# Kernel optimization log

Measured on AMD Instinct MI355X. Metric: run time of the kernel, lower is better.

The kernel has to match this reference:

```python
import jax, jax.numpy as jnp
import numpy as np

HOPS = 2
BN_EPS = 1e-5


def _glorot(key, shape):
    fan_in = shape[-2]
    bound = 1.0 / np.sqrt(fan_in)
    return jax.random.uniform(key, shape, jnp.float32, -bound, bound)


def setup_inputs() -> dict:
    key = jax.random.key(0)
    ks = jax.random.split(key, 12)
    n, e = 50000, 800000
    in_c, hid, out_c = 128, 96, 64
    x = jax.random.normal(ks[0], (n, in_c), jnp.float32)
    edge_index = jax.random.randint(ks[1], (2, e), 0, n, jnp.int32)
    # MixHopLayer 0: hops+1 linears in_c -> hid (stacked)
    conv0_W = _glorot(ks[2], (HOPS + 1, in_c, hid))
    conv0_b = jnp.zeros((HOPS + 1, hid), jnp.float32)
    # MixHopLayer 1: hops+1 linears hid*(hops+1) -> out_c
    conv1_W = _glorot(ks[3], (HOPS + 1, hid * (HOPS + 1), out_c))
    conv1_b = jnp.zeros((HOPS + 1, out_c), jnp.float32)
    # BatchNorm1d(hid*(hops+1)) eval-mode params/buffers
    w = hid * (HOPS + 1)
    bn_gamma = jnp.ones((w,), jnp.float32)
    bn_beta = jnp.zeros((w,), jnp.float32)
    bn_mean = 0.1 * jax.random.normal(ks[4], (w,), jnp.float32)
    bn_var = jnp.ones((w,), jnp.float32) + 0.1 * jax.random.uniform(ks[5], (w,))
    # final projection out_c*(hops+1) -> out_c
    fp_W = _glorot(ks[6], (out_c * (HOPS + 1), out_c))
    fp_b = jnp.zeros((out_c,), jnp.float32)
    return dict(x=x, edge_index=edge_index, conv0_W=conv0_W, conv0_b=conv0_b,
                conv1_W=conv1_W, conv1_b=conv1_b, bn_gamma=bn_gamma, bn_beta=bn_beta,
                bn_mean=bn_mean, bn_var=bn_var, fp_W=fp_W, fp_b=fp_b)


def _gcn_norm(edge_index, n):
    # PyG gcn_norm with add_self_loops=True, improved=False, symmetric norm.
    row, col = edge_index[0], edge_index[1]
    loop = jnp.arange(n, dtype=edge_index.dtype)
    row = jnp.concatenate([row, loop])
    col = jnp.concatenate([col, loop])
    deg = jax.ops.segment_sum(jnp.ones_like(col, jnp.float32), col, num_segments=n)
    dinv = jnp.where(deg > 0, jax.lax.rsqrt(deg), 0.0)
    w = dinv[row] * dinv[col]
    return row, col, w


def _spmm_adj_t(row, col, w, x, n):
    # adj_t = SparseTensor(row=col, col=row, value=w): out[col] += w * x[row]
    return jax.ops.segment_sum(w[:, None] * x[row], col, num_segments=n)


def _mixhop_layer(x, W, b, row, col, w, n):
    xs = [x @ W[0] + b[0]]
    for j in range(1, HOPS + 1):
        xj = x @ W[j] + b[j]
        for _ in range(j):
            xj = _spmm_adj_t(row, col, w, xj, n)
        xs.append(xj)
    return jnp.concatenate(xs, axis=1)


def reference(x, edge_index, conv0_W, conv0_b, conv1_W, conv1_b,
              bn_gamma, bn_beta, bn_mean, bn_var, fp_W, fp_b):
    n = x.shape[0]
    row, col, w = _gcn_norm(edge_index, n)
    h = _mixhop_layer(x, conv0_W, conv0_b, row, col, w, n)
    # BatchNorm1d (eval) + ReLU; dropout is identity in eval
    h = bn_gamma * (h - bn_mean) * jax.lax.rsqrt(bn_var + BN_EPS) + bn_beta
    h = jax.nn.relu(h)
    h = _mixhop_layer(h, conv1_W, conv1_b, row, col, w, n)
    return h @ fp_W + fp_b
```

## Files before the change

kernel.cpp:

```cpp
#include <hip/hip_runtime.h>

#define IN_C 128
#define HID 96
#define OUT_C 64
#define W0C 288
#define W1C 192
#define CAP 5120
#define EPB 4096

typedef __bf16 bf16x8v __attribute__((ext_vector_type(8)));
typedef float  f32x4v  __attribute__((ext_vector_type(4)));


__global__ void k_zero(int* __restrict__ p, int n) {
    int i = blockIdx.x * blockDim.x + threadIdx.x;
    if (i < n) p[i] = 0;
}

__global__ void k_count(const int* __restrict__ col, int* __restrict__ counts, int e) {
    int i = blockIdx.x * blockDim.x + threadIdx.x;
    if (i < e) atomicAdd(&counts[col[i]], 1);
}

__global__ void k_block_sum(const int* __restrict__ counts, int* __restrict__ bsums,
                            float* __restrict__ dinv, int n) {
    __shared__ int s[256];
    int i = blockIdx.x * 256 + threadIdx.x;
    int v = (i < n) ? counts[i] : 0;
    if (i < n) dinv[i] = rsqrtf((float)(v + 1));
    s[threadIdx.x] = v;
    __syncthreads();
    for (int off = 128; off > 0; off >>= 1) {
        if (threadIdx.x < (unsigned)off) s[threadIdx.x] += s[threadIdx.x + off];
        __syncthreads();
    }
    if (threadIdx.x == 0) bsums[blockIdx.x] = s[0];
}

__global__ void k_scan_bsums(int* __restrict__ bsums, int nb) {
    __shared__ int s[256];
    int v = ((int)threadIdx.x < nb) ? bsums[threadIdx.x] : 0;
    s[threadIdx.x] = v;
    __syncthreads();
    for (int off = 1; off < 256; off <<= 1) {
        int t = ((int)threadIdx.x >= off) ? s[threadIdx.x - off] : 0;
        __syncthreads();
        s[threadIdx.x] += t;
        __syncthreads();
    }
    if ((int)threadIdx.x < nb) bsums[threadIdx.x] = s[threadIdx.x] - v;
}

__global__ void k_row_ptr(const int* __restrict__ counts, const int* __restrict__ boffs,
                          int* __restrict__ row_ptr, int n) {
    __shared__ int s[256];
    int i = blockIdx.x * 256 + threadIdx.x;
    int v = (i < n) ? counts[i] : 0;
    s[threadIdx.x] = v;
    __syncthreads();
    for (int off = 1; off < 256; off <<= 1) {
        int t = ((int)threadIdx.x >= off) ? s[threadIdx.x - off] : 0;
        __syncthreads();
        s[threadIdx.x] += t;
        __syncthreads();
    }
    if (i < n) {
        row_ptr[i] = boffs[blockIdx.x] + s[threadIdx.x] - v;
        if (i == n - 1) row_ptr[n] = boffs[blockIdx.x] + s[threadIdx.x];
    }
}

__global__ __launch_bounds__(256) void k_binscatter(
        const int* __restrict__ row, const int* __restrict__ col,
        const int* __restrict__ row_ptr, int* __restrict__ bcur ,
        int2* __restrict__ binned, int e) {
    __shared__ int hist[256];
    __shared__ int base[256];
    int tid = threadIdx.x;
    int e0 = blockIdx.x * EPB;
    int cnt = min(EPB, e - e0);
    hist[tid] = 0;
    __syncthreads();
    int rr[16], cc[16], rk[16];
#pragma unroll
    for (int k = 0; k < 16; k++) {
        int idx = tid + k * 256;
        if (idx < cnt) {
            rr[k] = row[e0 + idx];
            cc[k] = col[e0 + idx];
            rk[k] = atomicAdd(&hist[cc[k] >> 8], 1);
        }
    }
    __syncthreads();
    {
        int h = hist[tid];
        if (h > 0) base[tid] = atomicAdd(&bcur[tid * 16], h);
    }
    __syncthreads();
#pragma unroll
    for (int k = 0; k < 16; k++) {
        int idx = tid + k * 256;
        if (idx < cnt) {
            int b = cc[k] >> 8;
            binned[row_ptr[b << 8] + base[b] + rk[k]] = make_int2(rr[k], cc[k]);
        }
    }
}

__global__ __launch_bounds__(256) void k_bucket_sort(
        const int2* __restrict__ binned, const int* __restrict__ row_ptr,
        const float* __restrict__ dinv,
        int* __restrict__ csr_src, float* __restrict__ csr_w, int n) {
    __shared__ int   s_src[CAP];
    __shared__ int   s_col[CAP];
    __shared__ int   s_ofs[256];
    __shared__ int   lcur[256];
    int tid = threadIdx.x;
    int node0 = blockIdx.x << 8;
    int nodeEnd = min(node0 + 256, n);
    int base = row_ptr[node0];
    int end  = row_ptr[nodeEnd];
    int cnt  = end - base;

    lcur[tid] = 0;
    __syncthreads();
    for (int t = tid; t < cnt; t += 256) {
        atomicAdd(&lcur[binned[base + t].x >> 8], 1);
    }
    __syncthreads();
    {
        int v = lcur[tid];
        s_ofs[tid] = v;
        __syncthreads();
        for (int o = 1; o < 256; o <<= 1) {
            int u = (tid >= o) ? s_ofs[tid - o] : 0;
            __syncthreads();
            s_ofs[tid] += u;
            __syncthreads();
        }
        lcur[tid] = s_ofs[tid] - v;
    }
    __syncthreads();
    for (int t = tid; t < cnt; t += 256) {
        int2 rc = binned[base + t];
        int pos = atomicAdd(&lcur[rc.x >> 8], 1);
        if (pos < CAP) {
            s_src[pos] = rc.x;
            s_col[pos] = rc.y;
        }
    }
    __syncthreads();
    {
        int node = node0 + tid;
        s_ofs[tid] = (node < n) ? (row_ptr[node] - base) : cnt;
        lcur[tid] = 0;
    }
    __syncthreads();
    int lim = min(cnt, CAP);
    for (int t = tid; t < lim; t += 256) {
        int r = s_src[t], c = s_col[t];
        int local = c - node0;
        int pos = s_ofs[local] + atomicAdd(&lcur[local], 1);
        csr_src[base + pos] = r;
        csr_w[base + pos]   = dinv[r] * dinv[c];
    }
}


__global__ void k_cvt_bf16(const float* __restrict__ src, __bf16* __restrict__ dst, int n8) {
    int i = blockIdx.x * blockDim.x + threadIdx.x;
    if (i >= n8) return;
    bf16x8v o;
#pragma unroll
    for (int q = 0; q < 8; q++) o[q] = (__bf16)src[i * 8 + q];
    *(bf16x8v*)(dst + (size_t)i * 8) = o;
}

__global__ void k_prep_all(const float* __restrict__ W0, const float* __restrict__ W1,
                           const float* __restrict__ Wf,
                           const float* __restrict__ gamma, const float* __restrict__ beta,
                           const float* __restrict__ mean, const float* __restrict__ var,
                           __bf16* __restrict__ w0t, __bf16* __restrict__ w1t,
                           __bf16* __restrict__ wft,
                           float* __restrict__ scale, float* __restrict__ shift) {
    const int T0 = 3 * IN_C * HID;
    const int T1 = 3 * W0C * OUT_C;
    const int T2 = W1C * OUT_C;
    int i = blockIdx.x * blockDim.x + threadIdx.x;
    if (i < T0) {
        int kn = IN_C * HID;
        int j = i / kn, r = i % kn;
        int k = r / HID, nn = r % HID;
        w0t[(size_t)j * kn + (size_t)nn * IN_C + k] = (__bf16)W0[i];
    } else if (i < T0 + T1) {
        int ii = i - T0;
        int kn = W0C * OUT_C;
        int j = ii / kn, r = ii % kn;
        int k = r / OUT_C, nn = r % OUT_C;
        w1t[(size_t)j * kn + (size_t)nn * W0C + k] = (__bf16)W1[ii];
    } else if (i < T0 + T1 + T2) {
        int ii = i - T0 - T1;
        int k = ii / OUT_C, nn = ii % OUT_C;
        wft[(size_t)nn * W1C + k] = (__bf16)Wf[ii];
    } else if (i < T0 + T1 + T2 + W0C) {
        int ii = i - T0 - T1 - T2;
        float s = gamma[ii] * rsqrtf(var[ii] + 1e-5f);
        scale[ii] = s;
        shift[ii] = beta[ii] - mean[ii] * s;
    }
}


__global__ __launch_bounds__(256) void k_mf_l0(
        const __bf16* __restrict__ xb, const __bf16* __restrict__ w0t ,
        const float* __restrict__ bias ,
        __bf16* __restrict__ h, __bf16* __restrict__ t12,
        const float* __restrict__ scale, const float* __restrict__ shift, int M) {
    const int RS = 104;
    __shared__ __bf16 tile[128 * RS];
    int tid = threadIdx.x;
    int wave = tid >> 6, lane = tid & 63;
    int ln = lane & 15, quad = lane >> 4;
    int j = blockIdx.y;
    int rowBase = blockIdx.x * 128;
    int waveRow = wave * 16;
    const __bf16* wjt = w0t + (size_t)j * HID * IN_C;
    f32x4v acc[2][6];
#pragma unroll
    for (int u = 0; u < 2; u++)
#pragma unroll
        for (int t = 0; t < 6; t++) acc[u][t] = (f32x4v){0.f, 0.f, 0.f, 0.f};
    const __bf16* arow0 = xb + (size_t)(rowBase + waveRow + ln) * IN_C + quad * 8;
    const __bf16* arow1 = arow0 + (size_t)64 * IN_C;
#pragma unroll
    for (int k = 0; k < 4; k++) {
        bf16x8v a0 = *(const bf16x8v*)(arow0 + k * 32);
        bf16x8v a1 = *(const bf16x8v*)(arow1 + k * 32);
#pragma unroll
        for (int c = 0; c < 6; c++) {
            bf16x8v b = *(const bf16x8v*)(wjt + (size_t)(c * 16 + ln) * IN_C + k * 32 + quad * 8);
            acc[0][c] = __builtin_amdgcn_mfma_f32_16x16x32_bf16(a0, b, acc[0][c], 0, 0, 0);
            acc[1][c] = __builtin_amdgcn_mfma_f32_16x16x32_bf16(a1, b, acc[1][c], 0, 0, 0);
        }
    }
    const float* bj = bias + j * HID;
    bool bn = (j == 0);
#pragma unroll
    for (int u = 0; u < 2; u++)
#pragma unroll
        for (int r = 0; r < 4; r++) {
            int lr = u * 64 + waveRow + quad * 4 + r;
#pragma unroll
            for (int c = 0; c < 6; c++) {
                int col = c * 16 + ln;
                float v = acc[u][c][r] + bj[col];
                if (bn) v = fmaxf(v * scale[col] + shift[col], 0.f);
                tile[lr * RS + col] = (__bf16)v;
            }
        }
    __syncthreads();
    __bf16* dst; int ld, c0;
    if (j == 0) { dst = h;   ld = W0C; c0 = 0; }
    else        { dst = t12; ld = 192; c0 = (j - 1) * 96; }
#pragma unroll
    for (int s = 0; s < 6; s++) {
        int idx = tid + s * 256;
        int r = idx / 12, c8 = idx % 12;
        int grow = rowBase + r;
        if (grow < M)
            *(bf16x8v*)(dst + (size_t)grow * ld + c0 + c8 * 8) =
                *(const bf16x8v*)(tile + r * RS + c8 * 8);
    }
}

__global__ __launch_bounds__(256) void k_mf_l1(
        const __bf16* __restrict__ hb, const __bf16* __restrict__ w1t ,
        const float* __restrict__ bias ,
        __bf16* __restrict__ g, __bf16* __restrict__ u12, int M) {
    const int RS = 72;
    __shared__ __bf16 tile[128 * RS];
    int tid = threadIdx.x;
    int wave = tid >> 6, lane = tid & 63;
    int ln = lane & 15, quad = lane >> 4;
    int j = blockIdx.y;
    int rowBase = blockIdx.x * 128;
    int waveRow = wave * 16;
    const __bf16* wjt = w1t + (size_t)j * OUT_C * W0C;
    f32x4v acc[2][4];
#pragma unroll
    for (int u = 0; u < 2; u++)
#pragma unroll
        for (int t = 0; t < 4; t++) acc[u][t] = (f32x4v){0.f, 0.f, 0.f, 0.f};
    const __bf16* arow0 = hb + (size_t)(rowBase + waveRow + ln) * W0C + quad * 8;
    const __bf16* arow1 = arow0 + (size_t)64 * W0C;
#pragma unroll
    for (int k = 0; k < 9; k++) {
        bf16x8v a0 = *(const bf16x8v*)(arow0 + k * 32);
        bf16x8v a1 = *(const bf16x8v*)(arow1 + k * 32);
#pragma unroll
        for (int c = 0; c < 4; c++) {
            bf16x8v b = *(const bf16x8v*)(wjt + (size_t)(c * 16 + ln) * W0C + k * 32 + quad * 8);
            acc[0][c] = __builtin_amdgcn_mfma_f32_16x16x32_bf16(a0, b, acc[0][c], 0, 0, 0);
            acc[1][c] = __builtin_amdgcn_mfma_f32_16x16x32_bf16(a1, b, acc[1][c], 0, 0, 0);
        }
    }
    const float* bj = bias + j * OUT_C;
#pragma unroll
    for (int u = 0; u < 2; u++)
#pragma unroll
        for (int r = 0; r < 4; r++) {
            int lr = u * 64 + waveRow + quad * 4 + r;
#pragma unroll
            for (int c = 0; c < 4; c++) {
                int col = c * 16 + ln;
                tile[lr * RS + col] = (__bf16)(acc[u][c][r] + bj[col]);
            }
        }
    __syncthreads();
    __bf16* dst; int ld, c0;
    if (j == 0) { dst = g;   ld = W1C; c0 = 0; }
    else        { dst = u12; ld = 128; c0 = (j - 1) * 64; }
#pragma unroll
    for (int s = 0; s < 4; s++) {
        int idx = tid + s * 256;
        int r = idx / 8, c8 = idx % 8;
        int grow = rowBase + r;
        if (grow < M)
            *(bf16x8v*)(dst + (size_t)grow * ld + c0 + c8 * 8) =
                *(const bf16x8v*)(tile + r * RS + c8 * 8);
    }
}

__global__ __launch_bounds__(256) void k_mf_fin(
        const __bf16* __restrict__ gb, const __bf16* __restrict__ wft ,
        const float* __restrict__ bias, float* __restrict__ out, int M) {
    const int RS = 68;
    __shared__ float tile[128 * RS];
    int tid = threadIdx.x;
    int wave = tid >> 6, lane = tid & 63;
    int ln = lane & 15, quad = lane >> 4;
    int rowBase = blockIdx.x * 128;
    int waveRow = wave * 16;
    f32x4v acc[2][4];
#pragma unroll
    for (int u = 0; u < 2; u++)
#pragma unroll
        for (int t = 0; t < 4; t++) acc[u][t] = (f32x4v){0.f, 0.f, 0.f, 0.f};
    const __bf16* arow0 = gb + (size_t)(rowBase + waveRow + ln) * W1C + quad * 8;
    const __bf16* arow1 = arow0 + (size_t)64 * W1C;
#pragma unroll
    for (int k = 0; k < 6; k++) {
        bf16x8v a0 = *(const bf16x8v*)(arow0 + k * 32);
        bf16x8v a1 = *(const bf16x8v*)(arow1 + k * 32);
#pragma unroll
        for (int c = 0; c < 4; c++) {
            bf16x8v b = *(const bf16x8v*)(wft + (size_t)(c * 16 + ln) * W1C + k * 32 + quad * 8);
            acc[0][c] = __builtin_amdgcn_mfma_f32_16x16x32_bf16(a0, b, acc[0][c], 0, 0, 0);
            acc[1][c] = __builtin_amdgcn_mfma_f32_16x16x32_bf16(a1, b, acc[1][c], 0, 0, 0);
        }
    }
#pragma unroll
    for (int u = 0; u < 2; u++)
#pragma unroll
        for (int r = 0; r < 4; r++) {
            int lr = u * 64 + waveRow + quad * 4 + r;
#pragma unroll
            for (int c = 0; c < 4; c++) {
                int col = c * 16 + ln;
                tile[lr * RS + col] = acc[u][c][r] + bias[col];
            }
        }
    __syncthreads();
#pragma unroll
    for (int s = 0; s < 8; s++) {
        int idx = tid + s * 256;
        int r = idx / 16, c4 = idx % 16;
        int grow = rowBase + r;
        if (grow < M)
            *(float4*)(out + (size_t)grow * OUT_C + c4 * 4) =
                *(const float4*)(tile + r * RS + c4 * 4);
    }
}

template <int C8, int NPB, bool BNRELU>
__global__ void k_spmm(const __bf16* __restrict__ xin, int ldx,
                       __bf16* __restrict__ xout, int ldo,
                       const int* __restrict__ row_ptr, const int* __restrict__ counts,
                       const int* __restrict__ csr_src, const float* __restrict__ csr_w,
                       const float* __restrict__ dinv, int n,
                       const float* __restrict__ scale, const float* __restrict__ shift,
                       int chan0) {
    int c8 = threadIdx.x % C8;
    int nl = threadIdx.x / C8;
    int node = blockIdx.x * NPB + nl;
    if (node >= n) return;
    float di = dinv[node];
    float lw = di * di;
    float acc[8];
    {
        bf16x8v v = *(const bf16x8v*)(xin + (size_t)node * ldx + c8 * 8);
#pragma unroll
        for (int q = 0; q < 8; q++) acc[q] = lw * (float)v[q];
    }
    int start = row_ptr[node];
    int cnt = counts[node];
    int k = 0;
    for (; k + 4 <= cnt; k += 4) {
        int s0 = csr_src[start + k + 0], s1 = csr_src[start + k + 1];
        int s2 = csr_src[start + k + 2], s3 = csr_src[start + k + 3];
        float w0 = csr_w[start + k + 0], w1 = csr_w[start + k + 1];
        float w2 = csr_w[start + k + 2], w3 = csr_w[start + k + 3];
        bf16x8v v0 = *(const bf16x8v*)(xin + (size_t)s0 * ldx + c8 * 8);
        bf16x8v v1 = *(const bf16x8v*)(xin + (size_t)s1 * ldx + c8 * 8);
        bf16x8v v2 = *(const bf16x8v*)(xin + (size_t)s2 * ldx + c8 * 8);
        bf16x8v v3 = *(const bf16x8v*)(xin + (size_t)s3 * ldx + c8 * 8);
#pragma unroll
        for (int q = 0; q < 8; q++)
            acc[q] += w0 * (float)v0[q] + w1 * (float)v1[q] +
                      w2 * (float)v2[q] + w3 * (float)v3[q];
    }
    for (; k < cnt; k++) {
        int src = csr_src[start + k];
        float w = csr_w[start + k];
        bf16x8v xv = *(const bf16x8v*)(xin + (size_t)src * ldx + c8 * 8);
#pragma unroll
        for (int q = 0; q < 8; q++) acc[q] += w * (float)xv[q];
    }
    bf16x8v o;
#pragma unroll
    for (int q = 0; q < 8; q++) {
        float v = acc[q];
        if (BNRELU) {
            int ch = chan0 + c8 * 8 + q;
            v = fmaxf(v * scale[ch] + shift[ch], 0.f);
        }
        o[q] = (__bf16)v;
    }
    *(bf16x8v*)(xout + (size_t)node * ldo + c8 * 8) = o;
}

template <int C8, int SPLIT, int NPB, bool BNA, bool BNB>
__global__ void k_spmm2(const __bf16* __restrict__ xin, int ldx,
                        __bf16* __restrict__ dstA, int ldA, int chanA,
                        __bf16* __restrict__ dstB, int ldB, int chanB,
                        const int* __restrict__ row_ptr, const int* __restrict__ counts,
                        const int* __restrict__ csr_src, const float* __restrict__ csr_w,
                        const float* __restrict__ dinv, int n,
                        const float* __restrict__ scale, const float* __restrict__ shift) {
    int c8 = threadIdx.x % C8;
    int nl = threadIdx.x / C8;
    int node = blockIdx.x * NPB + nl;
    if (node >= n) return;
    float di = dinv[node];
    float lw = di * di;
    float acc[8];
    {
        bf16x8v v = *(const bf16x8v*)(xin + (size_t)node * ldx + c8 * 8);
#pragma unroll
        for (int q = 0; q < 8; q++) acc[q] = lw * (float)v[q];
    }
    int start = row_ptr[node];
    int cnt = counts[node];
    int k = 0;
    for (; k + 4 <= cnt; k += 4) {
        int s0 = csr_src[start + k + 0], s1 = csr_src[start + k + 1];
        int s2 = csr_src[start + k + 2], s3 = csr_src[start + k + 3];
        float w0 = csr_w[start + k + 0], w1 = csr_w[start + k + 1];
        float w2 = csr_w[start + k + 2], w3 = csr_w[start + k + 3];
        bf16x8v v0 = *(const bf16x8v*)(xin + (size_t)s0 * ldx + c8 * 8);
        bf16x8v v1 = *(const bf16x8v*)(xin + (size_t)s1 * ldx + c8 * 8);
        bf16x8v v2 = *(const bf16x8v*)(xin + (size_t)s2 * ldx + c8 * 8);
        bf16x8v v3 = *(const bf16x8v*)(xin + (size_t)s3 * ldx + c8 * 8);
#pragma unroll
        for (int q = 0; q < 8; q++)
            acc[q] += w0 * (float)v0[q] + w1 * (float)v1[q] +
                      w2 * (float)v2[q] + w3 * (float)v3[q];
    }
    for (; k < cnt; k++) {
        int src = csr_src[start + k];
        float w = csr_w[start + k];
        bf16x8v xv = *(const bf16x8v*)(xin + (size_t)src * ldx + c8 * 8);
#pragma unroll
        for (int q = 0; q < 8; q++) acc[q] += w * (float)xv[q];
    }
    bool isA = c8 < SPLIT;
    __bf16* dst = isA ? dstA : dstB;
    int ld   = isA ? ldA : ldB;
    int lc8  = isA ? c8 : c8 - SPLIT;
    int chan = isA ? chanA : chanB;
    bool bn  = isA ? BNA : BNB;
    bf16x8v o;
#pragma unroll
    for (int q = 0; q < 8; q++) {
        float v = acc[q];
        if (bn) {
            int ch = chan + lc8 * 8 + q;
            v = fmaxf(v * scale[ch] + shift[ch], 0.f);
        }
        o[q] = (__bf16)v;
    }
    *(bf16x8v*)(dst + (size_t)node * ld + lc8 * 8) = o;
}


extern "C" void kernel_launch(void* const* d_in, const int* in_sizes, int n_in,
                              void* d_out, int out_size, void* d_ws, size_t ws_size,
                              hipStream_t stream) {
    const int n = in_sizes[0] / IN_C;
    const int e = in_sizes[1] / 2;

    const float* x    = (const float*)d_in[0];
    const int*   ei   = (const int*)d_in[1];
    const float* W0   = (const float*)d_in[2];
    const float* b0   = (const float*)d_in[3];
    const float* W1   = (const float*)d_in[4];
    const float* b1   = (const float*)d_in[5];
    const float* bn_g = (const float*)d_in[6];
    const float* bn_b = (const float*)d_in[7];
    const float* bn_m = (const float*)d_in[8];
    const float* bn_v = (const float*)d_in[9];
    const float* Wf   = (const float*)d_in[10];
    const float* bf   = (const float*)d_in[11];
    float* out = (float*)d_out;

    const int* e_row = ei;
    const int* e_col = ei + e;

    char* ws = (char*)d_ws;
    size_t off = 0;
    auto alloc = [&](size_t bytes) -> void* {
        void* p = ws + off;
        off += (bytes + 255) & ~(size_t)255;
        return p;
    };
    const int NP = n + 128;
    int*    counts  = (int*)alloc((size_t)(n + 256 * 16) * 4);
    int*    bcur    = counts + n;
    int*    row_ptr = (int*)alloc((size_t)(n + 1) * 4);
    int*    bsums   = (int*)alloc(256 * 4);
    float*  dinv    = (float*)alloc((size_t)n * 4);
    int2*   binned  = (int2*)alloc((size_t)e * 8);
    int*    csr_src = (int*)alloc((size_t)e * 4);
    float*  csr_w   = (float*)alloc((size_t)e * 4);
    float*  bnscale = (float*)alloc(W0C * 4);
    float*  bnshift = (float*)alloc(W0C * 4);
    __bf16* xb  = (__bf16*)alloc((size_t)NP * IN_C * 2);
    __bf16* w0t = (__bf16*)alloc((size_t)3 * HID * IN_C * 2);
    __bf16* w1t = (__bf16*)alloc((size_t)3 * OUT_C * W0C * 2);
    __bf16* wft = (__bf16*)alloc((size_t)OUT_C * W1C * 2);
    __bf16* t12 = (__bf16*)alloc((size_t)NP * 192 * 2);
    __bf16* tp  = (__bf16*)alloc((size_t)NP * HID * 2);
    __bf16* h   = (__bf16*)alloc((size_t)NP * W0C * 2);
    __bf16* g   = (__bf16*)alloc((size_t)NP * W1C * 2);
    __bf16* u12 = t12;
    __bf16* up  = tp;

    const int TB = 256;
    int nb = (n + 255) / 256;

    k_zero<<<dim3((n + 256 * 16 + TB - 1) / TB), dim3(TB), 0, stream>>>(counts, n + 256 * 16);
    k_count<<<dim3((e + TB - 1) / TB), dim3(TB), 0, stream>>>(e_col, counts, e);
    k_block_sum<<<dim3(nb), dim3(256), 0, stream>>>(counts, bsums, dinv, n);
    k_scan_bsums<<<dim3(1), dim3(256), 0, stream>>>(bsums, nb);
    k_row_ptr<<<dim3(nb), dim3(256), 0, stream>>>(counts, bsums, row_ptr, n);
    k_binscatter<<<dim3((e + EPB - 1) / EPB), dim3(256), 0, stream>>>(e_row, e_col, row_ptr,
                                                                      bcur, binned, e);
    k_bucket_sort<<<dim3(nb), dim3(256), 0, stream>>>(binned, row_ptr, dinv, csr_src, csr_w, n);

    k_cvt_bf16<<<dim3((n * IN_C / 8 + TB - 1) / TB), dim3(TB), 0, stream>>>(x, xb, n * IN_C / 8);
    int ptotal = 3 * IN_C * HID + 3 * W0C * OUT_C + W1C * OUT_C + W0C;
    k_prep_all<<<dim3((ptotal + TB - 1) / TB), dim3(TB), 0, stream>>>(
        W0, W1, Wf, bn_g, bn_b, bn_m, bn_v, w0t, w1t, wft, bnscale, bnshift);

    dim3 g128x3((n + 127) / 128, 3);
    dim3 g128((n + 127) / 128);

    k_mf_l0<<<g128x3, dim3(256), 0, stream>>>(xb, w0t, b0, h, t12, bnscale, bnshift, n);

    k_spmm2<24, 12, 8, true, false><<<dim3((n + 7) / 8), dim3(192), 0, stream>>>(
        t12, 192, h + HID, W0C, HID, tp, HID, 0,
        row_ptr, counts, csr_src, csr_w, dinv, n, bnscale, bnshift);
    k_spmm<12, 16, true><<<dim3((n + 15) / 16), dim3(192), 0, stream>>>(
        tp, HID, h + 2 * HID, W0C, row_ptr, counts, csr_src, csr_w, dinv, n,
        bnscale, bnshift, 2 * HID);

    k_mf_l1<<<g128x3, dim3(256), 0, stream>>>(h, w1t, b1, g, u12, n);

    k_spmm2<16, 8, 16, false, false><<<dim3((n + 15) / 16), dim3(256), 0, stream>>>(
        u12, 128, g + OUT_C, W1C, 0, up, OUT_C, 0,
        row_ptr, counts, csr_src, csr_w, dinv, n, nullptr, nullptr);
    k_spmm<8, 32, false><<<dim3((n + 31) / 32), dim3(256), 0, stream>>>(
        up, OUT_C, g + 2 * OUT_C, W1C, row_ptr, counts, csr_src, csr_w, dinv, n,
        nullptr, nullptr, 0);

    k_mf_fin<<<g128, dim3(256), 0, stream>>>(g, wft, bf, out, n);
}
```

Baseline: 362.0 us.

## Aggregate input features before projection in layer 0 and merge layer-1 GEMMs

Layer 0 now runs one sparse aggregation on the 128-wide input x (A·x) and applies the hop-1 and hop-2 weights afterwards. Bias is handled through precomputed per-node row sums of the normalized adjacency, accumulated in the bucket sort kernel. The old path ran a dual 96-wide SpMM on the projected features. The layer-1 GEMM is merged into a single kernel that computes all three weight slices from one load of the A rows, instead of using a 3-way grid. The intent is fewer sparse gathers and less repeated A-tile traffic, at the cost of more accumulator registers per thread and atomic float adds in shared memory.

After: 354.4 us. 1.02x faster.

```diff
diff --git a/kernel.cpp b/kernel.cpp
--- a/kernel.cpp
+++ b/kernel.cpp
@@ -110,11 +110,13 @@
 __global__ __launch_bounds__(256) void k_bucket_sort(
         const int2* __restrict__ binned, const int* __restrict__ row_ptr,
         const float* __restrict__ dinv,
-        int* __restrict__ csr_src, float* __restrict__ csr_w, int n) {
+        int* __restrict__ csr_src, float* __restrict__ csr_w,
+        float* __restrict__ arow, int n) {
     __shared__ int   s_src[CAP];
     __shared__ int   s_col[CAP];
     __shared__ int   s_ofs[256];
     __shared__ int   lcur[256];
+    __shared__ float s_a[256];
     int tid = threadIdx.x;
     int node0 = blockIdx.x << 8;
     int nodeEnd = min(node0 + 256, n);
@@ -154,6 +156,7 @@
         int node = node0 + tid;
         s_ofs[tid] = (node < n) ? (row_ptr[node] - base) : cnt;
         lcur[tid] = 0;
+        s_a[tid] = 0.f;
     }
     __syncthreads();
     int lim = min(cnt, CAP);
@@ -161,8 +164,18 @@
         int r = s_src[t], c = s_col[t];
         int local = c - node0;
         int pos = s_ofs[local] + atomicAdd(&lcur[local], 1);
+        float wv = dinv[r] * dinv[c];
         csr_src[base + pos] = r;
-        csr_w[base + pos]   = dinv[r] * dinv[c];
+        csr_w[base + pos]   = wv;
+        atomicAdd(&s_a[local], wv);
+    }
+    __syncthreads();
+    {
+        int node = node0 + tid;
+        if (node < n) {
+            float d = dinv[node];
+            arow[node] = s_a[tid] + d * d;
+        }
     }
 }
 
@@ -211,20 +224,18 @@
 }
 
 
-__global__ __launch_bounds__(256) void k_mf_l0(
+__global__ __launch_bounds__(256) void k_mf_l0a(
         const __bf16* __restrict__ xb, const __bf16* __restrict__ w0t ,
         const float* __restrict__ bias ,
-        __bf16* __restrict__ h, __bf16* __restrict__ t12,
+        __bf16* __restrict__ h,
         const float* __restrict__ scale, const float* __restrict__ shift, int M) {
     const int RS = 104;
     __shared__ __bf16 tile[128 * RS];
     int tid = threadIdx.x;
     int wave = tid >> 6, lane = tid & 63;
     int ln = lane & 15, quad = lane >> 4;
-    int j = blockIdx.y;
     int rowBase = blockIdx.x * 128;
     int waveRow = wave * 16;
-    const __bf16* wjt = w0t + (size_t)j * HID * IN_C;
     f32x4v acc[2][6];
 #pragma unroll
     for (int u = 0; u < 2; u++)
@@ -238,13 +249,11 @@
         bf16x8v a1 = *(const bf16x8v*)(arow1 + k * 32);
 #pragma unroll
         for (int c = 0; c < 6; c++) {
-            bf16x8v b = *(const bf16x8v*)(wjt + (size_t)(c * 16 + ln) * IN_C + k * 32 + quad * 8);
+            bf16x8v b = *(const bf16x8v*)(w0t + (size_t)(c * 16 + ln) * IN_C + k * 32 + quad * 8);
             acc[0][c] = __builtin_amdgcn_mfma_f32_16x16x32_bf16(a0, b, acc[0][c], 0, 0, 0);
             acc[1][c] = __builtin_amdgcn_mfma_f32_16x16x32_bf16(a1, b, acc[1][c], 0, 0, 0);
         }
     }
-    const float* bj = bias + j * HID;
-    bool bn = (j == 0);
 #pragma unroll
     for (int u = 0; u < 2; u++)
 #pragma unroll
@@ -253,27 +262,100 @@
 #pragma unroll
             for (int c = 0; c < 6; c++) {
                 int col = c * 16 + ln;
-                float v = acc[u][c][r] + bj[col];
-                if (bn) v = fmaxf(v * scale[col] + shift[col], 0.f);
+                float v = acc[u][c][r] + bias[col];
+                v = fmaxf(v * scale[col] + shift[col], 0.f);
                 tile[lr * RS + col] = (__bf16)v;
             }
         }
     __syncthreads();
-    __bf16* dst; int ld, c0;
-    if (j == 0) { dst = h;   ld = W0C; c0 = 0; }
-    else        { dst = t12; ld = 192; c0 = (j - 1) * 96; }
 #pragma unroll
     for (int s = 0; s < 6; s++) {
         int idx = tid + s * 256;
         int r = idx / 12, c8 = idx % 12;
         int grow = rowBase + r;
         if (grow < M)
-            *(bf16x8v*)(dst + (size_t)grow * ld + c0 + c8 * 8) =
+            *(bf16x8v*)(h + (size_t)grow * W0C + c8 * 8) =
                 *(const bf16x8v*)(tile + r * RS + c8 * 8);
     }
 }
 
-__global__ __launch_bounds__(256) void k_mf_l1(
+__global__ __launch_bounds__(256) void k_mf_l0b(
+        const __bf16* __restrict__ s1, const __bf16* __restrict__ w0t,
+        const float* __restrict__ bias , const float* __restrict__ arow,
+        __bf16* __restrict__ h, __bf16* __restrict__ tp,
+        const float* __restrict__ scale, const float* __restrict__ shift, int M) {
+    const int RS = 104;
+    __shared__ __bf16 tile[128 * RS];
+    int tid = threadIdx.x;
+    int wave = tid >> 6, lane = tid & 63;
+    int ln = lane & 15, quad = lane >> 4;
+    int rowBase = blockIdx.x * 128;
+    int waveRow = wave * 16;
+    const __bf16* w1p = w0t + (size_t)1 * HID * IN_C;
+    const __bf16* w2p = w0t + (size_t)2 * HID * IN_C;
+    f32x4v acc[2][2][6];
+#pragma unroll
+    for (int j = 0; j < 2; j++)
+#pragma unroll
+        for (int u = 0; u < 2; u++)
+#pragma unroll
+            for (int t = 0; t < 6; t++) acc[j][u][t] = (f32x4v){0.f, 0.f, 0.f, 0.f};
+    const __bf16* arow0 = s1 + (size_t)(rowBase + waveRow + ln) * IN_C + quad * 8;
+    const __bf16* arow1 = arow0 + (size_t)64 * IN_C;
+#pragma unroll
+    for (int k = 0; k < 4; k++) {
+        bf16x8v a0 = *(const bf16x8v*)(arow0 + k * 32);
+        bf16x8v a1 = *(const bf16x8v*)(arow1 + k * 32);
+#pragma unroll
+        for (int c = 0; c < 6; c++) {
+            bf16x8v b1 = *(const bf16x8v*)(w1p + (size_t)(c * 16 + ln) * IN_C + k * 32 + quad * 8);
+            bf16x8v b2 = *(const bf16x8v*)(w2p + (size_t)(c * 16 + ln) * IN_C + k * 32 + quad * 8);
+            acc[0][0][c] = __builtin_amdgcn_mfma_f32_16x16x32_bf16(a0, b1, acc[0][0][c], 0, 0, 0);
+            acc[0][1][c] = __builtin_amdgcn_mfma_f32_16x16x32_bf16(a1, b1, acc[0][1][c], 0, 0, 0);
+            acc[1][0][c] = __builtin_amdgcn_mfma_f32_16x16x32_bf16(a0, b2, acc[1][0][c], 0, 0, 0);
+            acc[1][1][c] = __builtin_amdgcn_mfma_f32_16x16x32_bf16(a1, b2, acc[1][1][c], 0, 0, 0);
+        }
+    }
+    float avs[2][4];
+#pragma unroll
+    for (int u = 0; u < 2; u++)
+#pragma unroll
+        for (int r = 0; r < 4; r++)
+            avs[u][r] = arow[rowBase + u * 64 + waveRow + quad * 4 + r];
+#pragma unroll
+    for (int jj = 0; jj < 2; jj++) {
+        const float* bj = bias + (jj + 1) * HID;
+#pragma unroll
+        for (int u = 0; u < 2; u++)
+#pragma unroll
+            for (int r = 0; r < 4; r++) {
+                int lr = u * 64 + waveRow + quad * 4 + r;
+                float av = avs[u][r];
+#pragma unroll
+                for (int c = 0; c < 6; c++) {
+                    int col = c * 16 + ln;
+                    float v = acc[jj][u][c][r] + av * bj[col];
+                    if (jj == 0) v = fmaxf(v * scale[HID + col] + shift[HID + col], 0.f);
+                    tile[lr * RS + col] = (__bf16)v;
+                }
+            }
+        __syncthreads();
+#pragma unroll
+        for (int s = 0; s < 6; s++) {
+            int idx = tid + s * 256;
+            int r = idx / 12, c8 = idx % 12;
+            int grow = rowBase + r;
+            if (grow < M) {
+                __bf16* dst = (jj == 0) ? (h + (size_t)grow * W0C + HID)
+                                        : (tp + (size_t)grow * HID);
+                *(bf16x8v*)(dst + c8 * 8) = *(const bf16x8v*)(tile + r * RS + c8 * 8);
+            }
+        }
+        __syncthreads();
+    }
+}
+
+__global__ __launch_bounds__(256) void k_mf_l1m(
         const __bf16* __restrict__ hb, const __bf16* __restrict__ w1t ,
         const float* __restrict__ bias ,
         __bf16* __restrict__ g, __bf16* __restrict__ u12, int M) {
@@ -282,15 +364,15 @@
     int tid = threadIdx.x;
     int wave = tid >> 6, lane = tid & 63;
     int ln = lane & 15, quad = lane >> 4;
-    int j = blockIdx.y;
     int rowBase = blockIdx.x * 128;
     int waveRow = wave * 16;
-    const __bf16* wjt = w1t + (size_t)j * OUT_C * W0C;
-    f32x4v acc[2][4];
-#pragma unroll
-    for (int u = 0; u < 2; u++)
-#pragma unroll
-        for (int t = 0; t < 4; t++) acc[u][t] = (f32x4v){0.f, 0.f, 0.f, 0.f};
+    f32x4v acc[3][2][4];
+#pragma unroll
+    for (int j = 0; j < 3; j++)
+#pragma unroll
+        for (int u = 0; u < 2; u++)
+#pragma unroll
+            for (int t = 0; t < 4; t++) acc[j][u][t] = (f32x4v){0.f, 0.f, 0.f, 0.f};
     const __bf16* arow0 = hb + (size_t)(rowBase + waveRow + ln) * W0C + quad * 8;
     const __bf16* arow1 = arow0 + (size_t)64 * W0C;
 #pragma unroll
@@ -299,35 +381,43 @@
         bf16x8v a1 = *(const bf16x8v*)(arow1 + k * 32);
 #pragma unroll
         for (int c = 0; c < 4; c++) {
-            bf16x8v b = *(const bf16x8v*)(wjt + (size_t)(c * 16 + ln) * W0C + k * 32 + quad * 8);
-            acc[0][c] = __builtin_amdgcn_mfma_f32_16x16x32_bf16(a0, b, acc[0][c], 0, 0, 0);
-            acc[1][c] = __builtin_amdgcn_mfma_f32_16x16x32_bf16(a1, b, acc[1][c], 0, 0, 0);
-        }
-    }
-    const float* bj = bias + j * OUT_C;
-#pragma unroll
-    for (int u = 0; u < 2; u++)
-#pragma unroll
-        for (int r = 0; r < 4; r++) {
-            int lr = u * 64 + waveRow + quad * 4 + r;
-#pragma unroll
-            for (int c = 0; c < 4; c++) {
-                int col = c * 16 + ln;
-                tile[lr * RS + col] = (__bf16)(acc[u][c][r] + bj[col]);
+#pragma unroll
+            for (int j = 0; j < 3; j++) {
+                bf16x8v b = *(const bf16x8v*)(w1t + (size_t)j * OUT_C * W0C +
+                                              (size_t)(c * 16 + ln) * W0C + k * 32 + quad * 8);
+                acc[j][0][c] = __builtin_amdgcn_mfma_f32_16x16x32_bf16(a0, b, acc[j][0][c], 0, 0, 0);
+                acc[j][1][c] = __builtin_amdgcn_mfma_f32_16x16x32_bf16(a1, b, acc[j][1][c], 0, 0, 0);
             }
         }
-    __syncthreads();
-    __bf16* dst; int ld, c0;
-    if (j == 0) { dst = g;   ld = W1C; c0 = 0; }
-    else        { dst = u12; ld = 128; c0 = (j - 1) * 64; }
-#pragma unroll
-    for (int s = 0; s < 4; s++) {
-        int idx = tid + s * 256;
-        int r = idx / 8, c8 = idx % 8;
-        int grow = rowBase + r;
-        if (grow < M)
-            *(bf16x8v*)(dst + (size_t)grow * ld + c0 + c8 * 8) =
-                *(const bf16x8v*)(tile + r * RS + c8 * 8);
+    }
+#pragma unroll
+    for (int j = 0; j < 3; j++) {
+        const float* bj = bias + j * OUT_C;
+#pragma unroll
+        for (int u = 0; u < 2; u++)
+#pragma unroll
+            for (int r = 0; r < 4; r++) {
+                int lr = u * 64 + waveRow + quad * 4 + r;
+#pragma unroll
+                for (int c = 0; c < 4; c++) {
+                    int col = c * 16 + ln;
+                    tile[lr * RS + col] = (__bf16)(acc[j][u][c][r] + bj[col]);
+                }
+            }
+        __syncthreads();
+        __bf16* dst = (j == 0) ? g : u12;
+        int ld = (j == 0) ? W1C : 128;
+        int c0 = (j == 2) ? OUT_C : 0;
+#pragma unroll
+        for (int s = 0; s < 4; s++) {
+            int idx = tid + s * 256;
+            int r = idx / 8, c8 = idx % 8;
+            int grow = rowBase + r;
+            if (grow < M)
+                *(bf16x8v*)(dst + (size_t)grow * ld + c0 + c8 * 8) =
+                    *(const bf16x8v*)(tile + r * RS + c8 * 8);
+        }
+        __syncthreads();
     }
 }
 
@@ -539,6 +629,7 @@
     int*    row_ptr = (int*)alloc((size_t)(n + 1) * 4);
     int*    bsums   = (int*)alloc(256 * 4);
     float*  dinv    = (float*)alloc((size_t)n * 4);
+    float*  arow    = (float*)alloc((size_t)NP * 4);
     int2*   binned  = (int2*)alloc((size_t)e * 8);
     int*    csr_src = (int*)alloc((size_t)e * 4);
     float*  csr_w   = (float*)alloc((size_t)e * 4);
@@ -548,11 +639,11 @@
     __bf16* w0t = (__bf16*)alloc((size_t)3 * HID * IN_C * 2);
     __bf16* w1t = (__bf16*)alloc((size_t)3 * OUT_C * W0C * 2);
     __bf16* wft = (__bf16*)alloc((size_t)OUT_C * W1C * 2);
-    __bf16* t12 = (__bf16*)alloc((size_t)NP * 192 * 2);
+    __bf16* s1  = (__bf16*)alloc((size_t)NP * 128 * 2);
     __bf16* tp  = (__bf16*)alloc((size_t)NP * HID * 2);
     __bf16* h   = (__bf16*)alloc((size_t)NP * W0C * 2);
     __bf16* g   = (__bf16*)alloc((size_t)NP * W1C * 2);
-    __bf16* u12 = t12;
+    __bf16* u12 = s1;
     __bf16* up  = tp;
 
     const int TB = 256;
@@ -565,26 +656,26 @@
     k_row_ptr<<<dim3(nb), dim3(256), 0, stream>>>(counts, bsums, row_ptr, n);
     k_binscatter<<<dim3((e + EPB - 1) / EPB), dim3(256), 0, stream>>>(e_row, e_col, row_ptr,
                                                                       bcur, binned, e);
-    k_bucket_sort<<<dim3(nb), dim3(256), 0, stream>>>(binned, row_ptr, dinv, csr_src, csr_w, n);
+    k_bucket_sort<<<dim3(nb), dim3(256), 0, stream>>>(binned, row_ptr, dinv,
+                                                      csr_src, csr_w, arow, n);
 
     k_cvt_bf16<<<dim3((n * IN_C / 8 + TB - 1) / TB), dim3(TB), 0, stream>>>(x, xb, n * IN_C / 8);
     int ptotal = 3 * IN_C * HID + 3 * W0C * OUT_C + W1C * OUT_C + W0C;
     k_prep_all<<<dim3((ptotal + TB - 1) / TB), dim3(TB), 0, stream>>>(
         W0, W1, Wf, bn_g, bn_b, bn_m, bn_v, w0t, w1t, wft, bnscale, bnshift);
 
-    dim3 g128x3((n + 127) / 128, 3);
     dim3 g128((n + 127) / 128);
 
-    k_mf_l0<<<g128x3, dim3(256), 0, stream>>>(xb, w0t, b0, h, t12, bnscale, bnshift, n);
-
-    k_spmm2<24, 12, 8, true, false><<<dim3((n + 7) / 8), dim3(192), 0, stream>>>(
-        t12, 192, h + HID, W0C, HID, tp, HID, 0,
-        row_ptr, counts, csr_src, csr_w, dinv, n, bnscale, bnshift);
+    k_mf_l0a<<<g128, dim3(256), 0, stream>>>(xb, w0t, b0, h, bnscale, bnshift, n);
+    k_spmm<16, 16, false><<<dim3((n + 15) / 16), dim3(256), 0, stream>>>(
+        xb, IN_C, s1, 128, row_ptr, counts, csr_src, csr_w, dinv, n,
+        nullptr, nullptr, 0);
+    k_mf_l0b<<<g128, dim3(256), 0, stream>>>(s1, w0t, b0, arow, h, tp, bnscale, bnshift, n);
     k_spmm<12, 16, true><<<dim3((n + 15) / 16), dim3(192), 0, stream>>>(
         tp, HID, h + 2 * HID, W0C, row_ptr, counts, csr_src, csr_w, dinv, n,
         bnscale, bnshift, 2 * HID);
 
-    k_mf_l1<<<g128x3, dim3(256), 0, stream>>>(h, w1t, b1, g, u12, n);
+    k_mf_l1m<<<g128, dim3(256), 0, stream>>>(h, w1t, b1, g, u12, n);
 
     k_spmm2<16, 8, 16, false, false><<<dim3((n + 15) / 16), dim3(256), 0, stream>>>(
         u12, 128, g + OUT_C, W1C, 0, up, OUT_C, 0,
```
